# Kernel tuning notes

Measured on AMD Instinct MI355X. Metric: run time of the kernel, lower is better.

## Reference

```python
import jax, jax.numpy as jnp
import numpy as np

N = 100000        # nodes
E = 1600000       # edges
F_IN = 32         # raw node features
C = 128           # out_channels / hidden
L = 5             # gated graph conv layers
G = 1024          # number of graphs in batch


def setup_inputs() -> dict:
    key = jax.random.key(0)
    ks = jax.random.split(key, 12)
    x = jax.random.normal(ks[0], (N, F_IN), dtype=jnp.float32)
    edge_index = jax.random.randint(ks[1], (2, E), 0, N, dtype=jnp.int32)
    edge_weight = jax.random.uniform(ks[2], (E,), dtype=jnp.float32)
    batch = jnp.sort(jax.random.randint(ks[3], (N,), 0, G, dtype=jnp.int32))
    # parameters (scaled small, fan-in style)
    W_emb = jax.random.normal(ks[4], (F_IN, C), dtype=jnp.float32) / np.sqrt(F_IN)
    b_emb = jnp.zeros((C,), dtype=jnp.float32)
    W = jax.random.normal(ks[5], (L, C, C), dtype=jnp.float32) / np.sqrt(C)
    W_ih = jax.random.normal(ks[6], (3 * C, C), dtype=jnp.float32) / np.sqrt(C)
    W_hh = jax.random.normal(ks[7], (3 * C, C), dtype=jnp.float32) / np.sqrt(C)
    b_ih = jnp.zeros((3 * C,), dtype=jnp.float32)
    b_hh = jnp.zeros((3 * C,), dtype=jnp.float32)
    W_prop = jax.random.normal(ks[8], (C, 1), dtype=jnp.float32) / np.sqrt(C)
    b_prop = jnp.zeros((1,), dtype=jnp.float32)
    return {"x": x, "edge_index": edge_index, "edge_weight": edge_weight,
            "batch": batch, "W_emb": W_emb, "b_emb": b_emb, "W": W,
            "W_ih": W_ih, "W_hh": W_hh, "b_ih": b_ih, "b_hh": b_hh,
            "W_prop": W_prop, "b_prop": b_prop}


def _gated_graph_conv(h, src, dst, edge_weight, W, W_ih, W_hh, b_ih, b_hh):
    n_nodes = h.shape[0]

    def step(h, Wl):
        m = h @ Wl                                    # [N,C] per-layer linear
        msg = m[src] * edge_weight[:, None]           # gather + edge weight [E,C]
        agg = jax.ops.segment_sum(msg, dst, num_segments=n_nodes)  # scatter-add
        # torch GRUCell (gate order r, z, n)
        gi = agg @ W_ih.T + b_ih                      # [N,3C]
        gh = h @ W_hh.T + b_hh
        i_r, i_z, i_n = jnp.split(gi, 3, axis=-1)
        h_r, h_z, h_n = jnp.split(gh, 3, axis=-1)
        r = jax.nn.sigmoid(i_r + h_r)
        z = jax.nn.sigmoid(i_z + h_z)
        n = jnp.tanh(i_n + r * h_n)
        h_new = (1.0 - z) * n + z * h
        return h_new, None

    h, _ = jax.lax.scan(step, h, W)
    return h


def reference(x, edge_index, edge_weight, batch, W_emb, b_emb, W,
              W_ih, W_hh, b_ih, b_hh, W_prop, b_prop):
    h0 = x @ W_emb + b_emb                            # node embedding [N,C]
    src, dst = edge_index[0], edge_index[1]
    h = _gated_graph_conv(h0, src, dst, edge_weight, W, W_ih, W_hh, b_ih, b_hh)
    node_prop = h @ W_prop + b_prop                   # [N,1]
    graph_prop = jax.ops.segment_sum(node_prop, batch, num_segments=G)  # [G,1]
    return graph_prop.squeeze(1)                      # [G]
```

## Files before the change

kernel.cpp:

```cpp
#include <hip/hip_runtime.h>

#define NN 100000
#define CC 128
#define EE 1600000
#define GG 1024
#define LL 5

typedef __attribute__((ext_vector_type(8))) short bf16x8;
typedef __attribute__((ext_vector_type(4))) float f32x4;

__device__ __forceinline__ float sigmoidf_(float x) { return 1.0f / (1.0f + __expf(-x)); }
__device__ __forceinline__ float tanhf_(float x) {
  float xx = fminf(15.0f, fmaxf(-15.0f, x));
  float t = __expf(-2.0f * xx);
  return (1.0f - t) / (1.0f + t);
}
__device__ __forceinline__ unsigned short f2bf(float x) {
  unsigned int u = __float_as_uint(x);
  return (unsigned short)((u + 0x7fffu + ((u >> 16) & 1u)) >> 16);
}
__device__ __forceinline__ float bflo(unsigned int u) { return __uint_as_float(u << 16); }
__device__ __forceinline__ float bfhi(unsigned int u) { return __uint_as_float(u & 0xffff0000u); }


__global__ __launch_bounds__(256) void pack_kernel(
    const float* __restrict__ src, unsigned short* __restrict__ dst)
{
  int t = blockIdx.x * 256 + threadIdx.x;
  int i = t & 7, l = (t >> 3) & 63, q = t >> 9;
  int ks = q & 3, cb = q >> 2;
  int k = ks * 32 + 8 * (l >> 4) + i;
  int c = cb * 16 + (l & 15);
  dst[t] = f2bf(src[(size_t)c * CC + k]);
}

__global__ __launch_bounds__(256) void fuse_pack_kernel(
    const float* __restrict__ Wl, const float* __restrict__ W_ih,
    unsigned short* __restrict__ dst)
{
  int t = blockIdx.x * 256 + threadIdx.x;
  int i = t & 7, l = (t >> 3) & 63, q = t >> 9;
  int ks = q & 3, cb = q >> 2;
  int k = ks * 32 + 8 * (l >> 4) + i;
  int c = cb * 16 + (l & 15);
  const float* wl = Wl + (size_t)k * CC;
  const float* wi = W_ih + (size_t)c * CC;
  float acc = 0.f;
  #pragma unroll 8
  for (int j = 0; j < CC; ++j) acc = fmaf(wl[j], wi[j], acc);
  dst[t] = f2bf(acc);
}


__global__ __launch_bounds__(256) void hist_kernel(const int* __restrict__ eidx,
                                                   int* __restrict__ deg)
{
  int e = blockIdx.x * blockDim.x + threadIdx.x;
  if (e < EE) atomicAdd(&deg[eidx[EE + e]], 1);
}

__global__ __launch_bounds__(256) void scan1_kernel(const int* __restrict__ deg,
                                                    int* __restrict__ bsum)
{
  __shared__ int red[4];
  int base = blockIdx.x * 1024 + threadIdx.x * 4;
  int s = 0;
  #pragma unroll
  for (int i = 0; i < 4; ++i) { int idx = base + i; if (idx < NN) s += deg[idx]; }
  #pragma unroll
  for (int off = 32; off; off >>= 1) s += __shfl_down(s, off, 64);
  if ((threadIdx.x & 63) == 0) red[threadIdx.x >> 6] = s;
  __syncthreads();
  if (threadIdx.x == 0) bsum[blockIdx.x] = red[0] + red[1] + red[2] + red[3];
}

__global__ void scan2_kernel(int* __restrict__ bsum, int nb)
{
  if (threadIdx.x == 0 && blockIdx.x == 0) {
    int acc = 0;
    for (int i = 0; i < nb; ++i) { int v = bsum[i]; bsum[i] = acc; acc += v; }
  }
}

__global__ __launch_bounds__(256) void scan3_kernel(const int* __restrict__ deg,
                                                    const int* __restrict__ bsum,
                                                    int* __restrict__ row_ptr,
                                                    int* __restrict__ cursor)
{
  __shared__ int ts[256];
  const int tid = threadIdx.x;
  const int base = blockIdx.x * 1024 + tid * 4;
  int v[4]; int s = 0;
  #pragma unroll
  for (int i = 0; i < 4; ++i) { int idx = base + i; v[i] = (idx < NN) ? deg[idx] : 0; s += v[i]; }
  ts[tid] = s; __syncthreads();
  for (int off = 1; off < 256; off <<= 1) {
    int t = (tid >= off) ? ts[tid - off] : 0;
    __syncthreads();
    ts[tid] += t;
    __syncthreads();
  }
  int excl = bsum[blockIdx.x] + ts[tid] - s;
  #pragma unroll
  for (int i = 0; i < 4; ++i) {
    int idx = base + i;
    if (idx < NN) { row_ptr[idx] = excl; cursor[idx] = excl; excl += v[i]; }
  }
  if (blockIdx.x == 0 && tid == 0) row_ptr[NN] = EE;
}

__global__ __launch_bounds__(256) void fill_kernel(const int* __restrict__ eidx,
                                                   const float* __restrict__ ew,
                                                   int* __restrict__ cursor,
                                                   int2* __restrict__ csr_sw)
{
  int e = blockIdx.x * blockDim.x + threadIdx.x;
  if (e < EE) {
    int d = eidx[EE + e];
    int p = atomicAdd(&cursor[d], 1);
    csr_sw[p] = make_int2(eidx[e], __float_as_int(ew[e]));
  }
}


__global__ __launch_bounds__(128) void embed_kernel(
    const float* __restrict__ x, const float* __restrict__ W_emb,
    const float* __restrict__ b_emb, float* __restrict__ h,
    unsigned short* __restrict__ h_bf)
{
  const int node = blockIdx.x;
  const int c = threadIdx.x;
  float acc = b_emb[c];
  #pragma unroll
  for (int k = 0; k < 32; ++k)
    acc = fmaf(x[node * 32 + k], W_emb[k * CC + c], acc);
  h[(size_t)node * CC + c] = acc;
  h_bf[(size_t)node * CC + c] = f2bf(acc);
}

__global__ __launch_bounds__(256) void aggregate_kernel(
    const unsigned short* __restrict__ h_bf, const int* __restrict__ row_ptr,
    const int2* __restrict__ csr_sw, unsigned short* __restrict__ agg_bf)
{
  const int lane = threadIdx.x & 63;
  const int node = (blockIdx.x * blockDim.x + threadIdx.x) >> 6;
  if (node >= NN) return;
  const int q = lane >> 4;
  const int t = lane & 15;
  const int beg = row_ptr[node], end = row_ptr[node + 1];

  float acc[8] = {0.f, 0.f, 0.f, 0.f, 0.f, 0.f, 0.f, 0.f};
  const int last = end - 1;

  for (int j = beg; j < end; j += 16) {
    const int e0 = j + q, e1 = j + 4 + q, e2 = j + 8 + q, e3 = j + 12 + q;
    const int i0 = min(e0, last), i1 = min(e1, last);
    const int i2 = min(e2, last), i3 = min(e3, last);
    const int2 r0 = csr_sw[i0], r1 = csr_sw[i1], r2 = csr_sw[i2], r3 = csr_sw[i3];
    const float w0 = (e0 < end) ? __int_as_float(r0.y) : 0.0f;
    const float w1 = (e1 < end) ? __int_as_float(r1.y) : 0.0f;
    const float w2 = (e2 < end) ? __int_as_float(r2.y) : 0.0f;
    const float w3 = (e3 < end) ? __int_as_float(r3.y) : 0.0f;
    const uint4 u0 = *(const uint4*)(h_bf + (size_t)r0.x * CC + t * 8);
    const uint4 u1 = *(const uint4*)(h_bf + (size_t)r1.x * CC + t * 8);
    const uint4 u2 = *(const uint4*)(h_bf + (size_t)r2.x * CC + t * 8);
    const uint4 u3 = *(const uint4*)(h_bf + (size_t)r3.x * CC + t * 8);
    acc[0] = fmaf(bflo(u0.x), w0, acc[0]); acc[1] = fmaf(bfhi(u0.x), w0, acc[1]);
    acc[2] = fmaf(bflo(u0.y), w0, acc[2]); acc[3] = fmaf(bfhi(u0.y), w0, acc[3]);
    acc[4] = fmaf(bflo(u0.z), w0, acc[4]); acc[5] = fmaf(bfhi(u0.z), w0, acc[5]);
    acc[6] = fmaf(bflo(u0.w), w0, acc[6]); acc[7] = fmaf(bfhi(u0.w), w0, acc[7]);
    acc[0] = fmaf(bflo(u1.x), w1, acc[0]); acc[1] = fmaf(bfhi(u1.x), w1, acc[1]);
    acc[2] = fmaf(bflo(u1.y), w1, acc[2]); acc[3] = fmaf(bfhi(u1.y), w1, acc[3]);
    acc[4] = fmaf(bflo(u1.z), w1, acc[4]); acc[5] = fmaf(bfhi(u1.z), w1, acc[5]);
    acc[6] = fmaf(bflo(u1.w), w1, acc[6]); acc[7] = fmaf(bfhi(u1.w), w1, acc[7]);
    acc[0] = fmaf(bflo(u2.x), w2, acc[0]); acc[1] = fmaf(bfhi(u2.x), w2, acc[1]);
    acc[2] = fmaf(bflo(u2.y), w2, acc[2]); acc[3] = fmaf(bfhi(u2.y), w2, acc[3]);
    acc[4] = fmaf(bflo(u2.z), w2, acc[4]); acc[5] = fmaf(bfhi(u2.z), w2, acc[5]);
    acc[6] = fmaf(bflo(u2.w), w2, acc[6]); acc[7] = fmaf(bfhi(u2.w), w2, acc[7]);
    acc[0] = fmaf(bflo(u3.x), w3, acc[0]); acc[1] = fmaf(bfhi(u3.x), w3, acc[1]);
    acc[2] = fmaf(bflo(u3.y), w3, acc[2]); acc[3] = fmaf(bfhi(u3.y), w3, acc[3]);
    acc[4] = fmaf(bflo(u3.z), w3, acc[4]); acc[5] = fmaf(bfhi(u3.z), w3, acc[5]);
    acc[6] = fmaf(bflo(u3.w), w3, acc[6]); acc[7] = fmaf(bfhi(u3.w), w3, acc[7]);
  }

  #pragma unroll
  for (int i = 0; i < 8; ++i) {
    acc[i] += __shfl_xor(acc[i], 16, 64);
    acc[i] += __shfl_xor(acc[i], 32, 64);
  }

  if (q == 0) {
    uint4 o;
    o.x = (unsigned)f2bf(acc[0]) | ((unsigned)f2bf(acc[1]) << 16);
    o.y = (unsigned)f2bf(acc[2]) | ((unsigned)f2bf(acc[3]) << 16);
    o.z = (unsigned)f2bf(acc[4]) | ((unsigned)f2bf(acc[5]) << 16);
    o.w = (unsigned)f2bf(acc[6]) | ((unsigned)f2bf(acc[7]) << 16);
    *(uint4*)(agg_bf + (size_t)node * CC + t * 8) = o;
  }
}

__global__ __launch_bounds__(256) void gru_kernel(
    const unsigned short* __restrict__ agg_bf, float* __restrict__ h,
    unsigned short* __restrict__ h_bf,
    const unsigned short* __restrict__ Wfuse_p, const unsigned short* __restrict__ Whh_p,
    const float* __restrict__ b_ih, const float* __restrict__ b_hh)
{
  const int lane = threadIdx.x & 63;
  const int wave = threadIdx.x >> 6;
  const int node0 = blockIdx.x * 128 + wave * 32;
  if (node0 >= NN) return;
  const int col16 = lane & 15, grp = lane >> 4;

  bf16x8 aA[2][4], aH[2][4];
  #pragma unroll
  for (int t = 0; t < 2; ++t) {
    const unsigned short* arow = agg_bf + (size_t)(node0 + t * 16 + col16) * CC + grp * 8;
    const unsigned short* hrow = h_bf  + (size_t)(node0 + t * 16 + col16) * CC + grp * 8;
    #pragma unroll
    for (int ks = 0; ks < 4; ++ks) {
      aA[t][ks] = *(const bf16x8*)(arow + ks * 32);
      aH[t][ks] = *(const bf16x8*)(hrow + ks * 32);
    }
  }

  const f32x4 z4 = {0.f, 0.f, 0.f, 0.f};

  #pragma unroll
  for (int cb = 0; cb < 8; ++cb) {
    f32x4 air[2] = {z4, z4}, ahr[2] = {z4, z4};
    f32x4 aiz[2] = {z4, z4}, ahz[2] = {z4, z4};
    f32x4 ain[2] = {z4, z4}, ahn[2] = {z4, z4};
    #pragma unroll
    for (int ks = 0; ks < 4; ++ks) {
      const size_t or_ = (size_t)((cb * 4 + ks) * 64 + lane) * 8;
      const size_t oz_ = (size_t)(((8 + cb) * 4 + ks) * 64 + lane) * 8;
      const size_t on_ = (size_t)(((16 + cb) * 4 + ks) * 64 + lane) * 8;
      bf16x8 bir = *(const bf16x8*)(Wfuse_p + or_);
      bf16x8 bhr = *(const bf16x8*)(Whh_p + or_);
      bf16x8 biz = *(const bf16x8*)(Wfuse_p + oz_);
      bf16x8 bhz = *(const bf16x8*)(Whh_p + oz_);
      bf16x8 bin = *(const bf16x8*)(Wfuse_p + on_);
      bf16x8 bhn = *(const bf16x8*)(Whh_p + on_);
      #pragma unroll
      for (int t = 0; t < 2; ++t) {
        air[t] = __builtin_amdgcn_mfma_f32_16x16x32_bf16(aA[t][ks], bir, air[t], 0, 0, 0);
        ahr[t] = __builtin_amdgcn_mfma_f32_16x16x32_bf16(aH[t][ks], bhr, ahr[t], 0, 0, 0);
        aiz[t] = __builtin_amdgcn_mfma_f32_16x16x32_bf16(aA[t][ks], biz, aiz[t], 0, 0, 0);
        ahz[t] = __builtin_amdgcn_mfma_f32_16x16x32_bf16(aH[t][ks], bhz, ahz[t], 0, 0, 0);
        ain[t] = __builtin_amdgcn_mfma_f32_16x16x32_bf16(aA[t][ks], bin, ain[t], 0, 0, 0);
        ahn[t] = __builtin_amdgcn_mfma_f32_16x16x32_bf16(aH[t][ks], bhn, ahn[t], 0, 0, 0);
      }
    }
    const int o = cb * 16 + col16;
    const float bir_ = b_ih[o],       bhr_ = b_hh[o];
    const float biz_ = b_ih[128 + o], bhz_ = b_hh[128 + o];
    const float bin_ = b_ih[256 + o], bhn_ = b_hh[256 + o];
    #pragma unroll
    for (int t = 0; t < 2; ++t) {
      #pragma unroll
      for (int r = 0; r < 4; ++r) {
        float rr = sigmoidf_(air[t][r] + ahr[t][r] + bir_ + bhr_);
        float zz = sigmoidf_(aiz[t][r] + ahz[t][r] + biz_ + bhz_);
        float nn = tanhf_(ain[t][r] + bin_ + rr * (ahn[t][r] + bhn_));
        size_t idx = (size_t)(node0 + t * 16 + grp * 4 + r) * CC + o;
        float hn = (1.0f - zz) * nn + zz * h[idx];
        h[idx] = hn;
        h_bf[idx] = f2bf(hn);
      }
    }
  }
}

__global__ __launch_bounds__(256) void prop_kernel(
    const float* __restrict__ h, const int* __restrict__ batch,
    const float* __restrict__ Wp, const float* __restrict__ bp,
    float* __restrict__ out)
{
  const int lane = threadIdx.x & 63;
  const int wid = (blockIdx.x * blockDim.x + threadIdx.x) >> 6;
  const int nw = (gridDim.x * blockDim.x) >> 6;
  for (int node = wid; node < NN; node += nw) {
    float v = h[(size_t)node * CC + lane] * Wp[lane]
            + h[(size_t)node * CC + 64 + lane] * Wp[64 + lane];
    #pragma unroll
    for (int off = 32; off > 0; off >>= 1) v += __shfl_down(v, off, 64);
    if (lane == 0) atomicAdd(&out[batch[node]], v + bp[0]);
  }
}

extern "C" void kernel_launch(void* const* d_in, const int* in_sizes, int n_in,
                              void* d_out, int out_size, void* d_ws, size_t ws_size,
                              hipStream_t stream)
{
  const float* x      = (const float*)d_in[0];
  const int*   eidx   = (const int*)d_in[1];
  const float* ew     = (const float*)d_in[2];
  const int*   batch  = (const int*)d_in[3];
  const float* W_emb  = (const float*)d_in[4];
  const float* b_emb  = (const float*)d_in[5];
  const float* W      = (const float*)d_in[6];
  const float* W_ih   = (const float*)d_in[7];
  const float* W_hh   = (const float*)d_in[8];
  const float* b_ih   = (const float*)d_in[9];
  const float* b_hh   = (const float*)d_in[10];
  const float* W_prop = (const float*)d_in[11];
  const float* b_prop = (const float*)d_in[12];
  float* out = (float*)d_out;

  char* p = (char*)d_ws;
  float* h              = (float*)p;          p += (size_t)NN * CC * sizeof(float);
  unsigned short* h_bf  = (unsigned short*)p; p += (size_t)NN * CC * sizeof(short);
  unsigned short* agg   = (unsigned short*)p; p += (size_t)NN * CC * sizeof(short);
  int2* csr_sw          = (int2*)p;           p += (size_t)EE * sizeof(int2);
  unsigned short* Wfuse_p = (unsigned short*)p; p += (size_t)LL * 49152 * sizeof(short);
  unsigned short* Whh_p = (unsigned short*)p; p += (size_t)49152 * sizeof(short);
  int* deg     = (int*)p;                     p += (size_t)(NN + 256) * sizeof(int);
  int* row_ptr = (int*)p;                     p += (size_t)(NN + 256) * sizeof(int);
  int* cursor  = (int*)p;                     p += (size_t)(NN + 256) * sizeof(int);
  int* bsum    = (int*)p;                     p += 1024 * sizeof(int);

  const int NB_SCAN = (NN + 1023) / 1024;
  const int EB = (EE + 255) / 256;
  const int MB2 = (NN + 127) / 128;

  pack_kernel<<<192, 256, 0, stream>>>(W_hh, Whh_p);
  for (int l = 0; l < LL; ++l)
    fuse_pack_kernel<<<192, 256, 0, stream>>>(W + (size_t)l * CC * CC, W_ih,
                                              Wfuse_p + (size_t)l * 49152);

  hipMemsetAsync(deg, 0, (size_t)NN * sizeof(int), stream);
  hist_kernel<<<EB, 256, 0, stream>>>(eidx, deg);
  scan1_kernel<<<NB_SCAN, 256, 0, stream>>>(deg, bsum);
  scan2_kernel<<<1, 64, 0, stream>>>(bsum, NB_SCAN);
  scan3_kernel<<<NB_SCAN, 256, 0, stream>>>(deg, bsum, row_ptr, cursor);
  fill_kernel<<<EB, 256, 0, stream>>>(eidx, ew, cursor, csr_sw);

  embed_kernel<<<NN, 128, 0, stream>>>(x, W_emb, b_emb, h, h_bf);

  for (int l = 0; l < LL; ++l) {
    aggregate_kernel<<<(NN + 3) / 4, 256, 0, stream>>>(h_bf, row_ptr, csr_sw, agg);
    gru_kernel<<<MB2, 256, 0, stream>>>(agg, h, h_bf,
                                        Wfuse_p + (size_t)l * 49152, Whh_p, b_ih, b_hh);
  }

  hipMemsetAsync(d_out, 0, (size_t)GG * sizeof(float), stream);
  prop_kernel<<<2048, 256, 0, stream>>>(h, batch, W_prop, b_prop, out);
}
```

Before: 947.4 us.

## Drop fp32 hidden state, merge pack/memset kernels, parallelize block scan

Removes the fp32 copy of the hidden state and keeps only bf16 h, staging each wave's h rows in LDS so the GRU blend reads them from shared memory instead of global fp32. The weight-packing kernels and both memsets are merged into one launch, and the serial scan2 becomes a wave-level shuffle scan. The prop kernel now reads bf16 h. This cuts global traffic and launch count, but the recurrent state loses precision across layers because it is rounded to bf16 each step.

```diff
diff --git a/kernel.cpp b/kernel.cpp
--- a/kernel.cpp
+++ b/kernel.cpp
@@ -21,34 +21,49 @@
 }
 __device__ __forceinline__ float bflo(unsigned int u) { return __uint_as_float(u << 16); }
 __device__ __forceinline__ float bfhi(unsigned int u) { return __uint_as_float(u & 0xffff0000u); }
-
-
-__global__ __launch_bounds__(256) void pack_kernel(
-    const float* __restrict__ src, unsigned short* __restrict__ dst)
-{
-  int t = blockIdx.x * 256 + threadIdx.x;
-  int i = t & 7, l = (t >> 3) & 63, q = t >> 9;
-  int ks = q & 3, cb = q >> 2;
-  int k = ks * 32 + 8 * (l >> 4) + i;
-  int c = cb * 16 + (l & 15);
-  dst[t] = f2bf(src[(size_t)c * CC + k]);
-}
-
-__global__ __launch_bounds__(256) void fuse_pack_kernel(
-    const float* __restrict__ Wl, const float* __restrict__ W_ih,
-    unsigned short* __restrict__ dst)
-{
-  int t = blockIdx.x * 256 + threadIdx.x;
-  int i = t & 7, l = (t >> 3) & 63, q = t >> 9;
-  int ks = q & 3, cb = q >> 2;
-  int k = ks * 32 + 8 * (l >> 4) + i;
-  int c = cb * 16 + (l & 15);
-  const float* wl = Wl + (size_t)k * CC;
-  const float* wi = W_ih + (size_t)c * CC;
-  float acc = 0.f;
-  #pragma unroll 8
-  for (int j = 0; j < CC; ++j) acc = fmaf(wl[j], wi[j], acc);
-  dst[t] = f2bf(acc);
+__device__ __forceinline__ float bf2f(unsigned short v) { return __uint_as_float((unsigned)v << 16); }
+
+#define PK_WHH 192
+#define PK_FUSE (192 * LL)
+#define PK_DEG ((NN + 256 + 255) / 256)
+#define PK_TOTAL (PK_WHH + PK_FUSE + PK_DEG + 1)
+
+__global__ __launch_bounds__(256) void pack_all_kernel(
+    const float* __restrict__ W, const float* __restrict__ W_ih,
+    const float* __restrict__ W_hh,
+    unsigned short* __restrict__ Whh_p, unsigned short* __restrict__ Wfuse_p,
+    int* __restrict__ deg, float* __restrict__ out)
+{
+  const int b = blockIdx.x;
+  const int tid = threadIdx.x;
+  if (b < PK_WHH) {
+    int t = b * 256 + tid;
+    int i = t & 7, l = (t >> 3) & 63, q = t >> 9;
+    int ks = q & 3, cb = q >> 2;
+    int k = ks * 32 + 8 * (l >> 4) + i;
+    int c = cb * 16 + (l & 15);
+    Whh_p[t] = f2bf(W_hh[(size_t)c * CC + k]);
+  } else if (b < PK_WHH + PK_FUSE) {
+    int idx = b - PK_WHH;
+    int layer = idx / 192;
+    int t = (idx % 192) * 256 + tid;
+    int i = t & 7, l = (t >> 3) & 63, q = t >> 9;
+    int ks = q & 3, cb = q >> 2;
+    int k = ks * 32 + 8 * (l >> 4) + i;
+    int c = cb * 16 + (l & 15);
+    const float* wl = W + (size_t)layer * CC * CC + (size_t)k * CC;
+    const float* wi = W_ih + (size_t)c * CC;
+    float acc = 0.f;
+    #pragma unroll 8
+    for (int j = 0; j < CC; ++j) acc = fmaf(wl[j], wi[j], acc);
+    Wfuse_p[(size_t)layer * 49152 + t] = f2bf(acc);
+  } else if (b < PK_WHH + PK_FUSE + PK_DEG) {
+    int i = (b - PK_WHH - PK_FUSE) * 256 + tid;
+    if (i < NN + 256) deg[i] = 0;
+  } else {
+    #pragma unroll
+    for (int i = 0; i < 4; ++i) out[i * 256 + tid] = 0.0f;
+  }
 }
 
 
@@ -74,11 +89,21 @@
   if (threadIdx.x == 0) bsum[blockIdx.x] = red[0] + red[1] + red[2] + red[3];
 }
 
-__global__ void scan2_kernel(int* __restrict__ bsum, int nb)
-{
-  if (threadIdx.x == 0 && blockIdx.x == 0) {
-    int acc = 0;
-    for (int i = 0; i < nb; ++i) { int v = bsum[i]; bsum[i] = acc; acc += v; }
+__global__ __launch_bounds__(64) void scan2_kernel(int* __restrict__ bsum, int nb)
+{
+  const int lane = threadIdx.x;
+  int carry = 0;
+  for (int base = 0; base < nb; base += 64) {
+    int i = base + lane;
+    int v = (i < nb) ? bsum[i] : 0;
+    const int orig = v;
+    #pragma unroll
+    for (int off = 1; off < 64; off <<= 1) {
+      int u = __shfl_up(v, off, 64);
+      if (lane >= off) v += u;
+    }
+    if (i < nb) bsum[i] = v - orig + carry;
+    carry += __shfl(v, 63, 64);
   }
 }
 
@@ -125,8 +150,7 @@
 
 __global__ __launch_bounds__(128) void embed_kernel(
     const float* __restrict__ x, const float* __restrict__ W_emb,
-    const float* __restrict__ b_emb, float* __restrict__ h,
-    unsigned short* __restrict__ h_bf)
+    const float* __restrict__ b_emb, unsigned short* __restrict__ h_bf)
 {
   const int node = blockIdx.x;
   const int c = threadIdx.x;
@@ -134,7 +158,6 @@
   #pragma unroll
   for (int k = 0; k < 32; ++k)
     acc = fmaf(x[node * 32 + k], W_emb[k * CC + c], acc);
-  h[(size_t)node * CC + c] = acc;
   h_bf[(size_t)node * CC + c] = f2bf(acc);
 }
 
@@ -200,26 +223,33 @@
 }
 
 __global__ __launch_bounds__(256) void gru_kernel(
-    const unsigned short* __restrict__ agg_bf, float* __restrict__ h,
-    unsigned short* __restrict__ h_bf,
+    const unsigned short* __restrict__ agg_bf, unsigned short* __restrict__ h_bf,
     const unsigned short* __restrict__ Wfuse_p, const unsigned short* __restrict__ Whh_p,
     const float* __restrict__ b_ih, const float* __restrict__ b_hh)
 {
+  __shared__ unsigned short hbuf[4][32][136];
   const int lane = threadIdx.x & 63;
   const int wave = threadIdx.x >> 6;
   const int node0 = blockIdx.x * 128 + wave * 32;
   if (node0 >= NN) return;
   const int col16 = lane & 15, grp = lane >> 4;
 
+  #pragma unroll
+  for (int i = 0; i < 8; ++i) {
+    const int chunk = lane + 64 * i;
+    const int row = chunk >> 4, c16 = chunk & 15;
+    uint4 v = *(const uint4*)(h_bf + (size_t)(node0 + row) * CC + c16 * 8);
+    *(uint4*)&hbuf[wave][row][c16 * 8] = v;
+  }
+
   bf16x8 aA[2][4], aH[2][4];
   #pragma unroll
   for (int t = 0; t < 2; ++t) {
     const unsigned short* arow = agg_bf + (size_t)(node0 + t * 16 + col16) * CC + grp * 8;
-    const unsigned short* hrow = h_bf  + (size_t)(node0 + t * 16 + col16) * CC + grp * 8;
     #pragma unroll
     for (int ks = 0; ks < 4; ++ks) {
       aA[t][ks] = *(const bf16x8*)(arow + ks * 32);
-      aH[t][ks] = *(const bf16x8*)(hrow + ks * 32);
+      aH[t][ks] = *(const bf16x8*)&hbuf[wave][t * 16 + col16][grp * 8 + ks * 32];
     }
   }
 
@@ -262,17 +292,16 @@
         float rr = sigmoidf_(air[t][r] + ahr[t][r] + bir_ + bhr_);
         float zz = sigmoidf_(aiz[t][r] + ahz[t][r] + biz_ + bhz_);
         float nn = tanhf_(ain[t][r] + bin_ + rr * (ahn[t][r] + bhn_));
-        size_t idx = (size_t)(node0 + t * 16 + grp * 4 + r) * CC + o;
-        float hn = (1.0f - zz) * nn + zz * h[idx];
-        h[idx] = hn;
-        h_bf[idx] = f2bf(hn);
+        const int row = t * 16 + grp * 4 + r;
+        float ho = bf2f(hbuf[wave][row][o]);
+        h_bf[(size_t)(node0 + row) * CC + o] = f2bf((1.0f - zz) * nn + zz * ho);
       }
     }
   }
 }
 
 __global__ __launch_bounds__(256) void prop_kernel(
-    const float* __restrict__ h, const int* __restrict__ batch,
+    const unsigned short* __restrict__ h_bf, const int* __restrict__ batch,
     const float* __restrict__ Wp, const float* __restrict__ bp,
     float* __restrict__ out)
 {
@@ -280,8 +309,8 @@
   const int wid = (blockIdx.x * blockDim.x + threadIdx.x) >> 6;
   const int nw = (gridDim.x * blockDim.x) >> 6;
   for (int node = wid; node < NN; node += nw) {
-    float v = h[(size_t)node * CC + lane] * Wp[lane]
-            + h[(size_t)node * CC + 64 + lane] * Wp[64 + lane];
+    unsigned int u = *(const unsigned int*)(h_bf + (size_t)node * CC + 2 * lane);
+    float v = bflo(u) * Wp[2 * lane] + bfhi(u) * Wp[2 * lane + 1];
     #pragma unroll
     for (int off = 32; off > 0; off >>= 1) v += __shfl_down(v, off, 64);
     if (lane == 0) atomicAdd(&out[batch[node]], v + bp[0]);
@@ -308,7 +337,6 @@
   float* out = (float*)d_out;
 
   char* p = (char*)d_ws;
-  float* h              = (float*)p;          p += (size_t)NN * CC * sizeof(float);
   unsigned short* h_bf  = (unsigned short*)p; p += (size_t)NN * CC * sizeof(short);
   unsigned short* agg   = (unsigned short*)p; p += (size_t)NN * CC * sizeof(short);
   int2* csr_sw          = (int2*)p;           p += (size_t)EE * sizeof(int2);
@@ -323,26 +351,21 @@
   const int EB = (EE + 255) / 256;
   const int MB2 = (NN + 127) / 128;
 
-  pack_kernel<<<192, 256, 0, stream>>>(W_hh, Whh_p);
-  for (int l = 0; l < LL; ++l)
-    fuse_pack_kernel<<<192, 256, 0, stream>>>(W + (size_t)l * CC * CC, W_ih,
-                                              Wfuse_p + (size_t)l * 49152);
-
-  hipMemsetAsync(deg, 0, (size_t)NN * sizeof(int), stream);
+  pack_all_kernel<<<PK_TOTAL, 256, 0, stream>>>(W, W_ih, W_hh, Whh_p, Wfuse_p, deg, out);
+
   hist_kernel<<<EB, 256, 0, stream>>>(eidx, deg);
   scan1_kernel<<<NB_SCAN, 256, 0, stream>>>(deg, bsum);
   scan2_kernel<<<1, 64, 0, stream>>>(bsum, NB_SCAN);
   scan3_kernel<<<NB_SCAN, 256, 0, stream>>>(deg, bsum, row_ptr, cursor);
   fill_kernel<<<EB, 256, 0, stream>>>(eidx, ew, cursor, csr_sw);
 
-  embed_kernel<<<NN, 128, 0, stream>>>(x, W_emb, b_emb, h, h_bf);
+  embed_kernel<<<NN, 128, 0, stream>>>(x, W_emb, b_emb, h_bf);
 
   for (int l = 0; l < LL; ++l) {
     aggregate_kernel<<<(NN + 3) / 4, 256, 0, stream>>>(h_bf, row_ptr, csr_sw, agg);
-    gru_kernel<<<MB2, 256, 0, stream>>>(agg, h, h_bf,
+    gru_kernel<<<MB2, 256, 0, stream>>>(agg, h_bf,
                                         Wfuse_p + (size_t)l * 49152, Whh_p, b_ih, b_hh);
   }
 
-  hipMemsetAsync(d_out, 0, (size_t)GG * sizeof(float), stream);
-  prop_kernel<<<2048, 256, 0, stream>>>(h, batch, W_prop, b_prop, out);
-}
+  prop_kernel<<<2048, 256, 0, stream>>>(h_bf, batch, W_prop, b_prop, out);
+}
```

New measurement: 881.4 us (median of 2 runs). 1.07x faster.
